# Kernel tuning notes

Measured on AMD Instinct MI355X. Metric: run time of the kernel, lower is better.

The kernel has to match this reference:

```python
import jax, jax.numpy as jnp
import numpy as np

B, T, V, F, H, WIN = 512, 49, 34, 16, 64, 4
W = T - WIN + 1  # 46 sliding windows


def make_pe(max_len, d):
    pos = np.arange(max_len, dtype=np.float32)[:, None]
    div = np.exp(np.arange(0, d, 2, dtype=np.float32) * (-np.log(10000.0) / d))
    pe = np.zeros((max_len, d), dtype=np.float32)
    pe[:, 0::2] = np.sin(pos * div)
    pe[:, 1::2] = np.cos(pos * div)
    return jnp.asarray(pe)


def impute(arr, delta_ts, mask, w, b):
    # arr/mask [B,T,V], delta_ts [B,T]; serial masked cumulative-sum + LOCF scan
    missing = (mask == 0).astype(arr.dtype)
    dd = jnp.broadcast_to(delta_ts[:, :, None], arr.shape)

    def step(carry, inp):
        c_prev, x_prev = carry
        d_t, x_t, m_t = inp
        c_t = d_t + c_prev * m_t                      # cum delta resets at observations
        x_new = jnp.where(m_t > 0, x_prev, x_t)       # last-observation carry-forward
        return (c_t, x_new), (c_t, x_new)

    xs = (dd.swapaxes(0, 1)[1:], arr.swapaxes(0, 1)[1:], missing.swapaxes(0, 1)[1:])
    _, (c_rest, x_rest) = jax.lax.scan(step, (dd[:, 0], arr[:, 0]), xs)
    cum = jnp.concatenate([dd[:, :1], c_rest.swapaxes(0, 1)], axis=1)
    last = jnp.concatenate([arr[:, :1], x_rest.swapaxes(0, 1)], axis=1)
    cum = cum / jnp.max(cum)
    decay = jnp.exp(-jnp.clip(w * cum + b, 0.0, 1000.0))  # w,b broadcast [1,V]
    means = jnp.mean(arr, axis=1, keepdims=True)
    return arr * mask + (1 - mask) * (decay * last + (1 - decay) * means)


def gru_layer(x, Wih, Whh, bih, bhh):
    # torch GRU gate order r,z,n; Wih [in,3H], Whh [H,3H]
    nB = x.shape[0]
    Hh = Whh.shape[0]
    xW = x @ Wih + bih  # [B,T,3H] precomputed input projections

    def step(h, xw_t):
        gh = h @ Whh + bhh
        xr, xz, xn = jnp.split(xw_t, 3, axis=-1)
        hr, hz, hn = jnp.split(gh, 3, axis=-1)
        r = jax.nn.sigmoid(xr + hr)
        z = jax.nn.sigmoid(xz + hz)
        n = jnp.tanh(xn + r * hn)
        h_new = (1 - z) * n + z * h
        return h_new, h_new

    _, ys = jax.lax.scan(step, jnp.zeros((nB, Hh), x.dtype), xW.swapaxes(0, 1))
    return ys.swapaxes(0, 1)


def forward(arr, mask, time, w_input_decay, b_input_decay,
            enc_W1, enc_b1, enc_W2, enc_b2,
            tla_Wq, tla_bq, tla_Wk, tla_bk, tla_Wv, tla_bv,
            adj, mp_W1, mp_b1, mp_W2, mp_b2,
            sa_Wq, sa_bq, sa_Wk, sa_bk, sa_Wv, sa_bv,
            gru_Wih0, gru_Whh0, gru_bih0, gru_bhh0,
            gru_Wih1, gru_Whh1, gru_bih1, gru_bhh1,
            ta_Wq, ta_bq, ta_Wk, ta_bk, ta_Wv, ta_bv,
            cls_W1, cls_b1, cls_W2, cls_b2):
    tt = time.T  # [B,T]
    delta = jnp.concatenate([jnp.zeros((tt.shape[0], 1), tt.dtype), tt[:, 1:] - tt[:, :-1]], axis=1)
    x = impute(arr, delta, mask, w_input_decay, b_input_decay)  # [B,T,V]
    # per-variable 2-layer MLP encoders (batched over V via einsum)
    inp = jnp.stack([x, mask], axis=-1)  # [B,T,V,2]
    h = jax.nn.relu(jnp.einsum('btvi,vif->btvf', inp, enc_W1) + enc_b1)
    enc = jnp.einsum('btvf,vfg->btvg', h, enc_W2) + enc_b2  # [B,T,V,F]
    # sliding windows (torch unfold + permute) + window positional encoding
    idx = jnp.arange(W)[:, None] + jnp.arange(WIN)[None, :]
    win = enc[:, idx] + make_pe(WIN, F)[None, None, :, None, :]
    xw = win.reshape(B * W, WIN, V, F)
    # TimeLagAttentionLayer: separate attention per variable, batched via einsum
    q = jnp.einsum('blvf,vfg->blvg', xw, tla_Wq) + tla_bq
    k = jnp.einsum('blvf,vfg->blvg', xw, tla_Wk) + tla_bk
    v = jnp.einsum('blvf,vfg->blvg', xw, tla_Wv) + tla_bv
    scores = jnp.einsum('blvg,bmvg->bvlm', q, k) / jnp.sqrt(jnp.asarray(F, xw.dtype))
    att = jax.nn.softmax(scores, axis=-1)
    att_out = jnp.einsum('bvlm,bmvf->bvf', att, v)  # (att @ v) then sum over lag dim
    # MessagePassingLayer
    message = jnp.einsum('uv,bvf->buf', adj, att_out)
    mp_out = jax.nn.relu(message @ mp_W1 + mp_b1) @ mp_W2 + mp_b2  # [B*W,V,1] (t_out path)
    _ = mp_out
    latent = message
    l_out = latent.reshape(B, W, V, F).transpose(0, 2, 3, 1)  # [B,V,F,W]
    # SignalAttentionLayer (faithful: permute to [B,V,W,F] then raw reshape to [B*W,V,F])
    xs = l_out + make_pe(V, F)[None, :, :, None]
    xs = xs.transpose(0, 1, 3, 2).reshape(B * W, V, F)
    Q = xs @ sa_Wq + sa_bq
    K = xs @ sa_Wk + sa_bk
    Vv = xs @ sa_Wv + sa_bv
    sw = jax.nn.softmax(jnp.einsum('bnd,bmd->bnm', Q, K) / jnp.sqrt(jnp.asarray(F, xs.dtype)), axis=-1)
    s_out = jnp.einsum('bnm,bmd->bd', sw, Vv).reshape(B, W, F)  # (w @ V).sum(dim=1)
    # 2-layer GRU predictor
    g1 = gru_layer(s_out, gru_Wih0, gru_Whh0, gru_bih0, gru_bhh0)
    g2 = gru_layer(g1, gru_Wih1, gru_Whh1, gru_bih1, gru_bhh1)  # [B,W,H]
    # TemporalAttention pooling
    xt = g2 + make_pe(W, H)[None]
    Qt = xt @ ta_Wq + ta_bq
    Kt = xt @ ta_Wk + ta_bk
    Vt = xt @ ta_Wv + ta_bv
    tw = jax.nn.softmax(jnp.einsum('bld,bmd->blm', Qt, Kt) / jnp.sqrt(jnp.asarray(H, xt.dtype)), axis=-1)
    t_val = jnp.einsum('blm,bmd->bd', tw, Vt)  # [B,H]
    pred = jax.nn.relu(t_val @ cls_W1 + cls_b1) @ cls_W2 + cls_b2  # [B,1]
    return pred


def setup_inputs():
    key = jax.random.key(0)
    ks = jax.random.split(key, 48)

    def rn(k, shape, s=0.1):
        return jax.random.normal(k, shape, jnp.float32) * s

    d = {}
    d['arr'] = jax.random.normal(ks[0], (B, T, V), jnp.float32)
    d['mask'] = (jax.random.uniform(ks[1], (B, T, V)) < 0.7).astype(jnp.float32)
    d['time'] = jnp.cumsum(jax.random.uniform(ks[2], (T, B), jnp.float32), axis=0)
    d['w_input_decay'] = jnp.full((1, V), 0.1, jnp.float32)
    d['b_input_decay'] = jnp.zeros((1, V), jnp.float32)
    d['enc_W1'] = rn(ks[3], (V, 2, F), 0.5); d['enc_b1'] = rn(ks[4], (V, F))
    d['enc_W2'] = rn(ks[5], (V, F, F), 0.25); d['enc_b2'] = rn(ks[6], (V, F))
    d['tla_Wq'] = rn(ks[7], (V, F, F), 0.25); d['tla_bq'] = rn(ks[8], (V, F))
    d['tla_Wk'] = rn(ks[9], (V, F, F), 0.25); d['tla_bk'] = rn(ks[10], (V, F))
    d['tla_Wv'] = rn(ks[11], (V, F, F), 0.25); d['tla_bv'] = rn(ks[12], (V, F))
    d['adj'] = jnp.eye(V, dtype=jnp.float32) + 0.2 * jnp.ones((V, V), jnp.float32)
    d['mp_W1'] = rn(ks[13], (F, F), 0.25); d['mp_b1'] = rn(ks[14], (F,))
    d['mp_W2'] = rn(ks[15], (F, 1), 0.25); d['mp_b2'] = rn(ks[16], (1,))
    d['sa_Wq'] = rn(ks[17], (F, F), 0.25); d['sa_bq'] = rn(ks[18], (F,))
    d['sa_Wk'] = rn(ks[19], (F, F), 0.25); d['sa_bk'] = rn(ks[20], (F,))
    d['sa_Wv'] = rn(ks[21], (F, F), 0.25); d['sa_bv'] = rn(ks[22], (F,))
    d['gru_Wih0'] = rn(ks[23], (F, 3 * H), 0.2); d['gru_Whh0'] = rn(ks[24], (H, 3 * H), 0.1)
    d['gru_bih0'] = rn(ks[25], (3 * H,)); d['gru_bhh0'] = rn(ks[26], (3 * H,))
    d['gru_Wih1'] = rn(ks[27], (H, 3 * H), 0.1); d['gru_Whh1'] = rn(ks[28], (H, 3 * H), 0.1)
    d['gru_bih1'] = rn(ks[29], (3 * H,)); d['gru_bhh1'] = rn(ks[30], (3 * H,))
    d['ta_Wq'] = rn(ks[31], (H, H), 0.12); d['ta_bq'] = rn(ks[32], (H,))
    d['ta_Wk'] = rn(ks[33], (H, H), 0.12); d['ta_bk'] = rn(ks[34], (H,))
    d['ta_Wv'] = rn(ks[35], (H, H), 0.12); d['ta_bv'] = rn(ks[36], (H,))
    d['cls_W1'] = rn(ks[37], (H, H), 0.12); d['cls_b1'] = rn(ks[38], (H,))
    d['cls_W2'] = rn(ks[39], (H, 1), 0.12); d['cls_b2'] = rn(ks[40], (1,))
    return d


def reference(arr, mask, time, w_input_decay, b_input_decay,
              enc_W1, enc_b1, enc_W2, enc_b2,
              tla_Wq, tla_bq, tla_Wk, tla_bk, tla_Wv, tla_bv,
              adj, mp_W1, mp_b1, mp_W2, mp_b2,
              sa_Wq, sa_bq, sa_Wk, sa_bk, sa_Wv, sa_bv,
              gru_Wih0, gru_Whh0, gru_bih0, gru_bhh0,
              gru_Wih1, gru_Whh1, gru_bih1, gru_bhh1,
              ta_Wq, ta_bq, ta_Wk, ta_bk, ta_Wv, ta_bv,
              cls_W1, cls_b1, cls_W2, cls_b2):
    return forward(arr, mask, time, w_input_decay, b_input_decay,
                   enc_W1, enc_b1, enc_W2, enc_b2,
                   tla_Wq, tla_bq, tla_Wk, tla_bk, tla_Wv, tla_bv,
                   adj, mp_W1, mp_b1, mp_W2, mp_b2,
                   sa_Wq, sa_bq, sa_Wk, sa_bk, sa_Wv, sa_bv,
                   gru_Wih0, gru_Whh0, gru_bih0, gru_bhh0,
                   gru_Wih1, gru_Whh1, gru_bih1, gru_bhh1,
                   ta_Wq, ta_bq, ta_Wk, ta_bk, ta_Wv, ta_bv,
                   cls_W1, cls_b1, cls_W2, cls_b2)
```

## Files before the change

kernel.cpp:

```cpp
#include <hip/hip_runtime.h>
#include <math.h>

#define BB 512
#define TT 49
#define VV 34
#define FF 16
#define HH 64
#define WW 46
#define BW (BB*WW)
#define TH3 (3*HH)
#define ROWS 25088
#define SG 2

#define SOUT_OFF   0ull
#define XW1_OFF    376832ull
#define G1_OFF     (XW1_OFF + 4521984ull)
#define XW2_OFF    (G1_OFF + 1507328ull)
#define G2_OFF     (XW2_OFF + 4521984ull)

#define MSG_SZ     12812288ull
#define CUM_SZ     852992ull
#define MEANS_SZ   17408ull
#define AO_OFF     12435456ull
#define MSG2_OFF   (AO_OFF + MSG_SZ)
#define CUM2_OFF   (MSG2_OFF + MSG_SZ)
#define LAST2_OFF  (CUM2_OFF + CUM_SZ)
#define MEANS2_OFF (LAST2_OFF + CUM_SZ)
#define MAX2_OFF   (MEANS2_OFF + MEANS_SZ)
#define PQ_OFF     (MAX2_OFF + 4ull)
#define SAW_OFF    (PQ_OFF + 6528ull)
#define FW_OFF     (SAW_OFF + 292ull)
#define WVIH_OFF   (FW_OFF + 27744ull)
#define BIAS2_OFF  (WVIH_OFF + 3072ull)

__global__ __launch_bounds__(256) void k_scan(
    const float* __restrict__ arr, const float* __restrict__ msk,
    const float* __restrict__ timeTB,
    float* __restrict__ cum, float* __restrict__ last,
    float* __restrict__ means, unsigned int* __restrict__ maxv) {
  int tid = blockIdx.x * 256 + threadIdx.x;
  int b = tid / VV, v = tid - b * VV;
  const int base = b * TT * VV + v;
  float x = arr[base];
  float c = 0.f, lm = 0.f, s = x;
  cum[base] = 0.f;
  last[base] = x;
  float tp = timeTB[b];
  for (int t = 1; t < TT; ++t) {
    float tc = timeTB[t * BB + b];
    float d = tc - tp; tp = tc;
    int e = base + t * VV;
    float a = arr[e], m = msk[e];
    float miss = (m == 0.f) ? 1.f : 0.f;
    c = d + c * miss;
    x = (miss > 0.f) ? x : a;
    cum[e] = c; last[e] = x;
    lm = fmaxf(lm, c);
    s += a;
  }
  means[tid] = s * (1.f / 49.f);
  #pragma unroll
  for (int off = 32; off; off >>= 1) lm = fmaxf(lm, __shfl_xor(lm, off));
  if ((threadIdx.x & 63) == 0) atomicMax(maxv, __float_as_uint(lm));
}

__global__ __launch_bounds__(256) void k_prep(
    const float* __restrict__ tlaWq, const float* __restrict__ tlaWk,
    const float* __restrict__ tlaWv,
    const float* __restrict__ tlaBq, const float* __restrict__ tlaBk,
    const float* __restrict__ tlaBv,
    const float* __restrict__ saWq, const float* __restrict__ saBq,
    const float* __restrict__ saWk, const float* __restrict__ saBk,
    const float* __restrict__ saWv, const float* __restrict__ saBv,
    const float* __restrict__ encW2, const float* __restrict__ encB2,
    const float* __restrict__ Wih0, const float* __restrict__ bih0,
    float* __restrict__ pqg, float* __restrict__ saw, float* __restrict__ fw,
    float* __restrict__ wvih, float* __restrict__ bias2) {
  const int bid = blockIdx.x;
  const int t = threadIdx.x;
  if (bid < 26) {
    int idx = bid * 256 + t;
    if (idx >= 6528) return;
    int which = idx / 2176;
    int r = idx - which * 2176;
    int l = r / 544;
    int rr = r - l * 544;
    int v = rr >> 4, f = rr & 15;
    const float* W = which == 0 ? tlaWq : which == 1 ? tlaWk : tlaWv;
    float acc = 0.f;
    #pragma unroll
    for (int i = 0; i < FF; ++i) {
      int i2 = i & ~1;
      float dv = expf(-logf(10000.f) * (float)i2 / (float)FF);
      float ang = (float)l * dv;
      float pe = (i & 1) ? cosf(ang) : sinf(ang);
      acc += pe * W[v * 256 + i * 16 + f];
    }
    pqg[idx] = acc;
  } else if (bid == 26) {
    int i = t & 15, j = t >> 4;
    float a = 0.f;
    #pragma unroll
    for (int f = 0; f < 16; ++f) a += saWq[i * 16 + f] * saWk[j * 16 + f];
    saw[j * 16 + i] = a;
    if (t < 16) {
      float pp = 0.f, qq = 0.f;
      #pragma unroll
      for (int f = 0; f < 16; ++f) { pp += saWq[t * 16 + f] * saBk[f]; qq += saWk[t * 16 + f] * saBq[f]; }
      saw[256 + t] = pp;
      saw[272 + t] = qq;
    }
    if (t == 0) {
      float c = 0.f;
      #pragma unroll
      for (int f = 0; f < 16; ++f) c += saBq[f] * saBk[f];
      saw[288] = c;
    }
  } else if (bid < 61) {
    const int v = bid - 27;
    const int f = t >> 4, o = t & 15;
    const float* W2v = encW2 + v * 256;
    float cq = 0.f, ck = 0.f, cv = 0.f;
    #pragma unroll
    for (int g = 0; g < 16; ++g) {
      float w2 = W2v[f * 16 + g];
      cq += w2 * tlaWq[v * 256 + g * 16 + o];
      ck += w2 * tlaWk[v * 256 + g * 16 + o];
      cv += w2 * tlaWv[v * 256 + g * 16 + o];
    }
    fw[v * 816 + 0 * 272 + f * 16 + o] = cq;
    fw[v * 816 + 1 * 272 + f * 16 + o] = ck;
    fw[v * 816 + 2 * 272 + f * 16 + o] = cv;
    if (t < 48) {
      int which = t >> 4, o2 = t & 15;
      const float* Wp = which == 0 ? tlaWq : which == 1 ? tlaWk : tlaWv;
      const float* Bp = which == 0 ? tlaBq : which == 1 ? tlaBk : tlaBv;
      float acc = Bp[v * 16 + o2];
      #pragma unroll
      for (int g = 0; g < 16; ++g) acc += encB2[v * 16 + g] * Wp[v * 256 + g * 16 + o2];
      fw[v * 816 + which * 272 + 256 + o2] = acc;
    }
  } else if (bid < 73) {
    int idx = (bid - 61) * 256 + t;
    int i = idx / 192, o = idx - i * 192;
    float acc = 0.f;
    #pragma unroll
    for (int f = 0; f < 16; ++f) acc += saWv[i * 16 + f] * Wih0[f * 192 + o];
    wvih[idx] = acc;
  } else {
    if (t < 192) {
      float acc = bih0[t];
      #pragma unroll
      for (int f = 0; f < 16; ++f) acc += 34.f * saBv[f] * Wih0[f * 192 + t];
      bias2[t] = acc;
    }
  }
}

__global__ __launch_bounds__(256) void k_enc4(
    const float* __restrict__ arr, const float* __restrict__ msk,
    const float* __restrict__ cum, const float* __restrict__ last,
    const float* __restrict__ means, const unsigned int* __restrict__ maxv,
    const float* __restrict__ wdec, const float* __restrict__ bdec,
    const float* __restrict__ W1, const float* __restrict__ B1,
    const float* __restrict__ fw, const float* __restrict__ pqg,
    float* __restrict__ ao) {
  __shared__ float pkv[4][3][TT * 17];
  const int v = blockIdx.x % VV;
  const int bgrp = blockIdx.x / VV;
  const int tid = threadIdx.x;
  const int wave = tid >> 6, lane = tid & 63;
  const int b = bgrp * 4 + wave;
  const float* fv = fw + v * 816;
  if (lane < TT) {
    const int t = lane;
    const int idx = (b * TT + t) * VV + v;
    float inv = 1.f / __uint_as_float(*maxv);
    float a = arr[idx], m = msk[idx];
    float cc = cum[idx] * inv;
    float ttc = fminf(fmaxf(wdec[v] * cc + bdec[v], 0.f), 1000.f);
    float dec = expf(-ttc);
    float xx = a * m + (1.f - m) * (dec * last[idx] + (1.f - dec) * means[b * VV + v]);
    float h[16];
    #pragma unroll
    for (int f = 0; f < 16; ++f)
      h[f] = fmaxf(xx * W1[v * 32 + f] + m * W1[v * 32 + 16 + f] + B1[v * 16 + f], 0.f);
    #pragma unroll
    for (int which = 0; which < 3; ++which) {
      const float* C = fv + which * 272;
      #pragma unroll
      for (int g = 0; g < 16; ++g) {
        float acc = C[256 + g];
        #pragma unroll
        for (int f = 0; f < 16; ++f) acc += h[f] * C[f * 16 + g];
        pkv[wave][which][t * 17 + g] = acc;
      }
    }
  }
  __syncthreads();
  if (lane < WW) {
    const int w = lane;
    const float* P = &pkv[wave][0][0];
    const float* K = &pkv[wave][1][0];
    const float* Vp = &pkv[wave][2][0];
    float kk[4][16];
    #pragma unroll
    for (int m = 0; m < 4; ++m)
      #pragma unroll
      for (int f = 0; f < 16; ++f)
        kk[m][f] = K[(w + m) * 17 + f] + pqg[2176 + m * 544 + v * 16 + f];
    float sc[4][4];
    #pragma unroll
    for (int l = 0; l < 4; ++l) {
      float qv[16];
      #pragma unroll
      for (int i = 0; i < 16; ++i)
        qv[i] = P[(w + l) * 17 + i] + pqg[l * 544 + v * 16 + i];
      #pragma unroll
      for (int m = 0; m < 4; ++m) {
        float s = 0.f;
        #pragma unroll
        for (int i = 0; i < 16; ++i) s += qv[i] * kk[m][i];
        sc[l][m] = s * 0.25f;
      }
    }
    float csum[4] = {0.f, 0.f, 0.f, 0.f};
    #pragma unroll
    for (int l = 0; l < 4; ++l) {
      float mx = fmaxf(fmaxf(sc[l][0], sc[l][1]), fmaxf(sc[l][2], sc[l][3]));
      float sum = 0.f;
      #pragma unroll
      for (int m = 0; m < 4; ++m) { sc[l][m] = expf(sc[l][m] - mx); sum += sc[l][m]; }
      float r = 1.f / sum;
      #pragma unroll
      for (int m = 0; m < 4; ++m) csum[m] += sc[l][m] * r;
    }
    float outv[16];
    #pragma unroll
    for (int f = 0; f < 16; ++f) outv[f] = 0.f;
    #pragma unroll
    for (int m = 0; m < 4; ++m) {
      float c = csum[m];
      #pragma unroll
      for (int f = 0; f < 16; ++f)
        outv[f] += c * (Vp[(w + m) * 17 + f] + pqg[2 * 2176 + m * 544 + v * 16 + f]);
    }
    float4* d4 = (float4*)(ao + ((size_t)(b * VV + v) * WW + w) * 16);
    #pragma unroll
    for (int j = 0; j < 4; ++j)
      d4[j] = make_float4(outv[4*j], outv[4*j+1], outv[4*j+2], outv[4*j+3]);
  }
}

#define MPW 12
__global__ __launch_bounds__(256) void k_mp(
    const float* __restrict__ ao, const float* __restrict__ adj,
    float* __restrict__ msg2) {
  __shared__ float adjs[VV * VV];
  __shared__ __align__(16) float aos[VV][MPW * 16];
  __shared__ float pes[VV * 16];
  const int bb = blockIdx.x >> 2;
  const int wt = blockIdx.x & 3;
  const int w0 = wt * MPW;
  const int wc = (wt == 3) ? (WW - 3 * MPW) : MPW;
  const int tid = threadIdx.x;
  for (int i = tid; i < VV * VV; i += 256) adjs[i] = adj[i];
  for (int i = tid; i < VV * 16; i += 256) {
    int u = i >> 4, f = i & 15;
    int f2 = f & ~1;
    float dv = expf(-logf(10000.f) * (float)f2 / 16.f);
    float ang = (float)u * dv;
    pes[i] = (f & 1) ? cosf(ang) : sinf(ang);
  }
  const int nq = wc * 4;
  for (int i = tid; i < VV * nq; i += 256) {
    int vv2 = i / nq, r = i - vv2 * nq;
    int wl = r >> 2, q = r & 3;
    float4 val = *(const float4*)(ao + ((size_t)(bb * VV + vv2) * WW + w0 + wl) * 16 + q * 4);
    *(float4*)&aos[vv2][wl * 16 + q * 4] = val;
  }
  __syncthreads();
  for (int i = tid; i < VV * nq; i += 256) {
    int u = i / nq, r = i - u * nq;
    int wl = r >> 2, q = r & 3;
    float a0 = 0.f, a1 = 0.f, a2 = 0.f, a3 = 0.f;
    for (int vv2 = 0; vv2 < VV; ++vv2) {
      float a = adjs[u * VV + vv2];
      float4 s = *(const float4*)&aos[vv2][wl * 16 + q * 4];
      a0 += a * s.x; a1 += a * s.y; a2 += a * s.z; a3 += a * s.w;
    }
    float4 o = make_float4(a0 + pes[u * 16 + q * 4],
                           a1 + pes[u * 16 + q * 4 + 1],
                           a2 + pes[u * 16 + q * 4 + 2],
                           a3 + pes[u * 16 + q * 4 + 3]);
    *(float4*)(msg2 + ((size_t)(bb * VV + u) * WW + w0 + wl) * 16 + q * 4) = o;
  }
}

#define DOT4(a,b) ((a).x*(b).x + (a).y*(b).y + (a).z*(b).z + (a).w*(b).w)
__global__ __launch_bounds__(256) void k_sa4(
    const float* __restrict__ msg2, const float* __restrict__ saw,
    const float* __restrict__ wvih, const float* __restrict__ bias2,
    float* __restrict__ xw1) {
  __shared__ float As[256];
  __shared__ float ps[16], q2s[16];
  __shared__ __align__(16) float xs[SG][36][20];
  __shared__ __align__(16) float zs[SG][36][20];
  __shared__ float sc[SG][36][37];
  __shared__ float uws[SG][36], vws[SG][36];
  __shared__ float rs[SG][34], cs[SG][34];
  __shared__ float ys[SG][16];
  __shared__ float c0s;
  const int tid = threadIdx.x;
  const int n0 = blockIdx.x * SG;
  As[tid] = saw[tid];
  if (tid < 16) { ps[tid] = saw[256 + tid]; q2s[tid] = saw[272 + tid]; }
  if (tid == 0) c0s = saw[288];
  {
    const float4* src = (const float4*)(msg2 + (size_t)n0 * 544);
    for (int i = tid; i < SG * 136; i += 256) {
      int g = i / 136, r = i - g * 136;
      int m = r >> 2, q = r & 3;
      ((float4*)&xs[g][m][0])[q] = src[i];
    }
  }
  __syncthreads();
  for (int idx = tid; idx < SG * 136; idx += 256) {
    int g = idx / 136, r = idx - g * 136;
    int m0 = (r >> 3) * 2, i0 = (r & 7) * 2;
    float z00 = 0.f, z01 = 0.f, z10 = 0.f, z11 = 0.f;
    #pragma unroll
    for (int jc = 0; jc < 4; ++jc) {
      float4 xa = ((const float4*)&xs[g][m0][0])[jc];
      float4 xb = ((const float4*)&xs[g][m0 + 1][0])[jc];
      #pragma unroll
      for (int jj = 0; jj < 4; ++jj) {
        int j = jc * 4 + jj;
        float xj0 = (jj == 0) ? xa.x : (jj == 1) ? xa.y : (jj == 2) ? xa.z : xa.w;
        float xj1 = (jj == 0) ? xb.x : (jj == 1) ? xb.y : (jj == 2) ? xb.z : xb.w;
        float a0 = As[j * 16 + i0], a1 = As[j * 16 + i0 + 1];
        z00 += a0 * xj0; z01 += a1 * xj0; z10 += a0 * xj1; z11 += a1 * xj1;
      }
    }
    zs[g][m0][i0] = z00; zs[g][m0][i0 + 1] = z01;
    zs[g][m0 + 1][i0] = z10; zs[g][m0 + 1][i0 + 1] = z11;
  }
  if (tid < SG * 34) {
    int g = tid / 34, m = tid - g * 34;
    float pu = 0.f, pv = 0.f;
    #pragma unroll
    for (int i = 0; i < 16; ++i) { float x = xs[g][m][i]; pu += x * ps[i]; pv += x * q2s[i]; }
    uws[g][m] = pu; vws[g][m] = pv;
  }
  __syncthreads();
  for (int idx = tid; idx < SG * 81; idx += 256) {
    int g = idx / 81, r = idx - g * 81;
    int l0 = (r / 9) * 4, m0 = (r - (r / 9) * 9) * 4;
    float s00=0,s01=0,s02=0,s03=0, s10=0,s11=0,s12=0,s13=0;
    float s20=0,s21=0,s22=0,s23=0, s30=0,s31=0,s32=0,s33=0;
    #pragma unroll
    for (int ic = 0; ic < 4; ++ic) {
      float4 x0 = ((const float4*)&xs[g][l0 + 0][0])[ic];
      float4 x1 = ((const float4*)&xs[g][l0 + 1][0])[ic];
      float4 x2 = ((const float4*)&xs[g][l0 + 2][0])[ic];
      float4 x3 = ((const float4*)&xs[g][l0 + 3][0])[ic];
      float4 z0 = ((const float4*)&zs[g][m0 + 0][0])[ic];
      float4 z1 = ((const float4*)&zs[g][m0 + 1][0])[ic];
      float4 z2 = ((const float4*)&zs[g][m0 + 2][0])[ic];
      float4 z3 = ((const float4*)&zs[g][m0 + 3][0])[ic];
      s00 += DOT4(x0,z0); s01 += DOT4(x0,z1); s02 += DOT4(x0,z2); s03 += DOT4(x0,z3);
      s10 += DOT4(x1,z0); s11 += DOT4(x1,z1); s12 += DOT4(x1,z2); s13 += DOT4(x1,z3);
      s20 += DOT4(x2,z0); s21 += DOT4(x2,z1); s22 += DOT4(x2,z2); s23 += DOT4(x2,z3);
      s30 += DOT4(x3,z0); s31 += DOT4(x3,z1); s32 += DOT4(x3,z2); s33 += DOT4(x3,z3);
    }
    float c0 = c0s;
    float u0 = uws[g][l0], u1 = uws[g][l0+1], u2 = uws[g][l0+2], u3 = uws[g][l0+3];
    float v0 = vws[g][m0], v1 = vws[g][m0+1], v2 = vws[g][m0+2], v3 = vws[g][m0+3];
    sc[g][l0+0][m0+0] = (s00+u0+v0+c0)*0.25f; sc[g][l0+0][m0+1] = (s01+u0+v1+c0)*0.25f;
    sc[g][l0+0][m0+2] = (s02+u0+v2+c0)*0.25f; sc[g][l0+0][m0+3] = (s03+u0+v3+c0)*0.25f;
    sc[g][l0+1][m0+0] = (s10+u1+v0+c0)*0.25f; sc[g][l0+1][m0+1] = (s11+u1+v1+c0)*0.25f;
    sc[g][l0+1][m0+2] = (s12+u1+v2+c0)*0.25f; sc[g][l0+1][m0+3] = (s13+u1+v3+c0)*0.25f;
    sc[g][l0+2][m0+0] = (s20+u2+v0+c0)*0.25f; sc[g][l0+2][m0+1] = (s21+u2+v1+c0)*0.25f;
    sc[g][l0+2][m0+2] = (s22+u2+v2+c0)*0.25f; sc[g][l0+2][m0+3] = (s23+u2+v3+c0)*0.25f;
    sc[g][l0+3][m0+0] = (s30+u3+v0+c0)*0.25f; sc[g][l0+3][m0+1] = (s31+u3+v1+c0)*0.25f;
    sc[g][l0+3][m0+2] = (s32+u3+v2+c0)*0.25f; sc[g][l0+3][m0+3] = (s33+u3+v3+c0)*0.25f;
  }
  __syncthreads();
  if (tid < SG * 34) {
    int g = tid / 34, l = tid - g * 34;
    float mx = -1e30f;
    for (int m = 0; m < 34; ++m) mx = fmaxf(mx, sc[g][l][m]);
    float sum = 0.f;
    for (int m = 0; m < 34; ++m) { float e = expf(sc[g][l][m] - mx); sc[g][l][m] = e; sum += e; }
    rs[g][l] = 1.f / sum;
  }
  __syncthreads();
  if (tid < SG * 34) {
    int g = tid / 34, m = tid - g * 34;
    float acc = 0.f;
    for (int l = 0; l < 34; ++l) acc += sc[g][l][m] * rs[g][l];
    cs[g][m] = acc;
  }
  __syncthreads();
  if (tid < SG * 16) {
    int g = tid >> 4, i = tid & 15;
    float acc = 0.f;
    for (int m = 0; m < 34; ++m) acc += cs[g][m] * xs[g][m][i];
    ys[g][i] = acc;
  }
  __syncthreads();
  for (int idx = tid; idx < SG * 192; idx += 256) {
    int g = idx / 192, o = idx - g * 192;
    float acc = bias2[o];
    #pragma unroll
    for (int i = 0; i < 16; ++i) acc += ys[g][i] * wvih[i * 192 + o];
    xw1[(size_t)(n0 + g) * 192 + o] = acc;
  }
}

#define RL(x,i) __uint_as_float(__builtin_amdgcn_readlane(__float_as_uint(x), (i)))
__global__ __launch_bounds__(64) void k_gru2(
    const float* __restrict__ xw, const float* __restrict__ Whh,
    const float* __restrict__ bhh, float* __restrict__ gout) {
  const int tid = threadIdx.x;
  const int b = blockIdx.x;
  float wr[64], wz[64], wn[64];
  #pragma unroll
  for (int i = 0; i < 64; ++i) {
    wr[i] = Whh[i * 192 + tid];
    wz[i] = Whh[i * 192 + 64 + tid];
    wn[i] = Whh[i * 192 + 128 + tid];
  }
  const float br = bhh[tid], bz = bhh[64 + tid], bn = bhh[128 + tid];
  float h = 0.f;
  const float* xr = xw + (size_t)b * WW * 192;
  for (int w = 0; w < WW; ++w, xr += 192) {
    float xrv = xr[tid], xzv = xr[64 + tid], xnv = xr[128 + tid];
    float pr0 = br, pr1 = 0.f, pr2 = 0.f, pr3 = 0.f;
    float pz0 = bz, pz1 = 0.f, pz2 = 0.f, pz3 = 0.f;
    float pn0 = bn, pn1 = 0.f, pn2 = 0.f, pn3 = 0.f;
    #pragma unroll
    for (int i = 0; i < 64; i += 4) {
      float h0 = RL(h, i), h1 = RL(h, i + 1), h2 = RL(h, i + 2), h3 = RL(h, i + 3);
      pr0 += h0 * wr[i];     pr1 += h1 * wr[i + 1];
      pr2 += h2 * wr[i + 2]; pr3 += h3 * wr[i + 3];
      pz0 += h0 * wz[i];     pz1 += h1 * wz[i + 1];
      pz2 += h2 * wz[i + 2]; pz3 += h3 * wz[i + 3];
      pn0 += h0 * wn[i];     pn1 += h1 * wn[i + 1];
      pn2 += h2 * wn[i + 2]; pn3 += h3 * wn[i + 3];
    }
    float ar = (pr0 + pr1) + (pr2 + pr3);
    float az = (pz0 + pz1) + (pz2 + pz3);
    float an = (pn0 + pn1) + (pn2 + pn3);
    float r = 1.f / (1.f + expf(-(xrv + ar)));
    float z = 1.f / (1.f + expf(-(xzv + az)));
    float n = tanhf(xnv + r * an);
    h = (1.f - z) * n + z * h;
    gout[((size_t)b * WW + w) * HH + tid] = h;
  }
}

__global__ __launch_bounds__(192) void k_xw2(
    const float* __restrict__ x, const float* __restrict__ Wih,
    const float* __restrict__ bih, float* __restrict__ xw) {
  __shared__ float xsh[16][HH];
  int n0 = blockIdx.x * 16;
  int tid = threadIdx.x;
  for (int idx = tid; idx < 16 * HH; idx += 192) {
    int ns = idx >> 6, i = idx & 63;
    xsh[ns][i] = x[(size_t)(n0 + ns) * HH + i];
  }
  __syncthreads();
  float acc[16];
  float bb = bih[tid];
  #pragma unroll
  for (int ns = 0; ns < 16; ++ns) acc[ns] = bb;
  for (int i = 0; i < HH; ++i) {
    float wv = Wih[i * TH3 + tid];
    #pragma unroll
    for (int ns = 0; ns < 16; ++ns) acc[ns] += xsh[ns][i] * wv;
  }
  #pragma unroll
  for (int ns = 0; ns < 16; ++ns) xw[(size_t)(n0 + ns) * TH3 + tid] = acc[ns];
}

__global__ __launch_bounds__(256) void k_ta(
    const float* __restrict__ g2,
    const float* __restrict__ Wq, const float* __restrict__ bq,
    const float* __restrict__ Wk, const float* __restrict__ bk,
    const float* __restrict__ Wv, const float* __restrict__ bv,
    const float* __restrict__ cW1, const float* __restrict__ cb1,
    const float* __restrict__ cW2, const float* __restrict__ cb2,
    float* __restrict__ out) {
  __shared__ float xt[WW * 65];
  __shared__ float QKVs[3][WW * 65];
  __shared__ float sc[WW * WW];
  __shared__ float cs[WW];
  __shared__ float tval[HH];
  __shared__ float hrelu[HH];
  int tid = threadIdx.x;
  int b = blockIdx.x;
  for (int idx = tid; idx < WW * HH; idx += 256) {
    int w = idx >> 6, d = idx & 63;
    int f2 = d & ~1;
    float dv = expf(-logf(10000.f) * (float)f2 / (float)HH);
    float ang = (float)w * dv;
    float pe = (d & 1) ? cosf(ang) : sinf(ang);
    xt[w * 65 + d] = g2[(size_t)(b * WW + w) * HH + d] + pe;
  }
  __syncthreads();
  if (tid < 192) {
    int which = tid >> 6, d = tid & 63;
    const float* Wt = which == 0 ? Wq : which == 1 ? Wk : Wv;
    float bias = (which == 0 ? bq : which == 1 ? bk : bv)[d];
    float col[HH];
    #pragma unroll
    for (int i = 0; i < HH; ++i) col[i] = Wt[i * HH + d];
    float* dst = &QKVs[which][0];
    for (int w = 0; w < WW; ++w) {
      float acc = bias;
      #pragma unroll
      for (int i = 0; i < HH; ++i) acc += xt[w * 65 + i] * col[i];
      dst[w * 65 + d] = acc;
    }
  }
  __syncthreads();
  for (int idx = tid; idx < WW * WW; idx += 256) {
    int l = idx / WW, m = idx - l * WW;
    float s = 0.f;
    #pragma unroll
    for (int i = 0; i < HH; ++i) s += QKVs[0][l * 65 + i] * QKVs[1][m * 65 + i];
    sc[idx] = s * 0.125f;
  }
  __syncthreads();
  if (tid < WW) {
    float mx = -1e30f;
    for (int m = 0; m < WW; ++m) mx = fmaxf(mx, sc[tid * WW + m]);
    float sum = 0.f;
    for (int m = 0; m < WW; ++m) { float e = expf(sc[tid * WW + m] - mx); sc[tid * WW + m] = e; sum += e; }
    float r = 1.f / sum;
    for (int m = 0; m < WW; ++m) sc[tid * WW + m] *= r;
  }
  __syncthreads();
  if (tid < WW) {
    float s = 0.f;
    for (int l = 0; l < WW; ++l) s += sc[l * WW + tid];
    cs[tid] = s;
  }
  __syncthreads();
  if (tid < HH) {
    float acc = 0.f;
    for (int m = 0; m < WW; ++m) acc += cs[m] * QKVs[2][m * 65 + tid];
    tval[tid] = acc;
  }
  __syncthreads();
  if (tid < HH) {
    float acc = cb1[tid];
    #pragma unroll
    for (int d = 0; d < HH; ++d) acc += tval[d] * cW1[d * HH + tid];
    hrelu[tid] = fmaxf(acc, 0.f);
  }
  __syncthreads();
  if (tid == 0) {
    float acc = cb2[0];
    for (int j = 0; j < HH; ++j) acc += hrelu[j] * cW2[j];
    out[b] = acc;
  }
}

extern "C" void kernel_launch(void* const* d_in, const int* in_sizes, int n_in,
                              void* d_out, int out_size, void* d_ws, size_t ws_size,
                              hipStream_t stream) {
  (void)in_sizes; (void)n_in; (void)out_size; (void)ws_size;
  const float* arr    = (const float*)d_in[0];
  const float* msk    = (const float*)d_in[1];
  const float* timeTB = (const float*)d_in[2];
  const float* wdec   = (const float*)d_in[3];
  const float* bdec   = (const float*)d_in[4];
  const float* encW1  = (const float*)d_in[5];
  const float* encB1  = (const float*)d_in[6];
  const float* encW2  = (const float*)d_in[7];
  const float* encB2  = (const float*)d_in[8];
  const float* tlaWq  = (const float*)d_in[9];
  const float* tlaBq  = (const float*)d_in[10];
  const float* tlaWk  = (const float*)d_in[11];
  const float* tlaBk  = (const float*)d_in[12];
  const float* tlaWv  = (const float*)d_in[13];
  const float* tlaBv  = (const float*)d_in[14];
  const float* adj    = (const float*)d_in[15];
  const float* saWq   = (const float*)d_in[20];
  const float* saBq   = (const float*)d_in[21];
  const float* saWk   = (const float*)d_in[22];
  const float* saBk   = (const float*)d_in[23];
  const float* saWv   = (const float*)d_in[24];
  const float* saBv   = (const float*)d_in[25];
  const float* gWih0  = (const float*)d_in[26];
  const float* gWhh0  = (const float*)d_in[27];
  const float* gBih0  = (const float*)d_in[28];
  const float* gBhh0  = (const float*)d_in[29];
  const float* gWih1  = (const float*)d_in[30];
  const float* gWhh1  = (const float*)d_in[31];
  const float* gBih1  = (const float*)d_in[32];
  const float* gBhh1  = (const float*)d_in[33];
  const float* taWq   = (const float*)d_in[34];
  const float* taBq   = (const float*)d_in[35];
  const float* taWk   = (const float*)d_in[36];
  const float* taBk   = (const float*)d_in[37];
  const float* taWv   = (const float*)d_in[38];
  const float* taBv   = (const float*)d_in[39];
  const float* cW1    = (const float*)d_in[40];
  const float* cb1    = (const float*)d_in[41];
  const float* cW2    = (const float*)d_in[42];
  const float* cb2    = (const float*)d_in[43];
  float* out = (float*)d_out;
  float* ws  = (float*)d_ws;

  float* ao    = ws + AO_OFF;
  float* msg2  = ws + MSG2_OFF;
  float* cum   = ws + CUM2_OFF;
  float* last  = ws + LAST2_OFF;
  float* means = ws + MEANS2_OFF;
  unsigned int* maxv = (unsigned int*)(ws + MAX2_OFF);
  float* pqg   = ws + PQ_OFF;
  float* saw   = ws + SAW_OFF;
  float* fw    = ws + FW_OFF;
  float* wvih  = ws + WVIH_OFF;
  float* bias2 = ws + BIAS2_OFF;

  float* xw1  = ws + XW1_OFF;
  float* g1   = ws + G1_OFF;
  float* xw2  = ws + XW2_OFF;
  float* g2   = ws + G2_OFF;

  hipMemsetAsync(maxv, 0, sizeof(unsigned int), stream);
  k_scan<<<68, 256, 0, stream>>>(arr, msk, timeTB, cum, last, means, maxv);
  k_prep<<<74, 256, 0, stream>>>(tlaWq, tlaWk, tlaWv, tlaBq, tlaBk, tlaBv,
                                 saWq, saBq, saWk, saBk, saWv, saBv,
                                 encW2, encB2, gWih0, gBih0,
                                 pqg, saw, fw, wvih, bias2);
  k_enc4<<<VV * 128, 256, 0, stream>>>(arr, msk, cum, last, means, maxv,
                                       wdec, bdec, encW1, encB1, fw, pqg, ao);
  k_mp<<<BB * 4, 256, 0, stream>>>(ao, adj, msg2);
  k_sa4<<<BW / SG, 256, 0, stream>>>(msg2, saw, wvih, bias2, xw1);
  k_gru2<<<BB, 64, 0, stream>>>(xw1, gWhh0, gBhh0, g1);
  k_xw2<<<BW / 16, 192, 0, stream>>>(g1, gWih1, gBih1, xw2);
  k_gru2<<<BB, 64, 0, stream>>>(xw2, gWhh1, gBhh1, g2);
  k_ta<<<BB, 256, 0, stream>>>(g2, taWq, taBq, taWk, taBk, taWv, taBv,
                               cW1, cb1, cW2, cb2, out);
}
```

Measured before the change: 347.1 us.

## Restructure spatial attention kernel to one wavefront per window with register rows

Replaces the SG=2 shared-memory tiled spatial-attention kernel with a version that handles four windows per block, one wavefront per window. Each lane owns one query row: it computes the projected row z, the scores against all 34 keys and the softmax entirely in registers, then writes only the normalized probabilities to LDS. Weights are read directly from global memory (uniform loads) instead of being staged in shared memory. This cuts block count and barrier-separated phases, and fuses the softmax normalization into the score loop. In exchange, lanes 34-63 sit idle during most phases and register pressure rises from the 16+34 float arrays per lane.

```diff
diff --git a/kernel.cpp b/kernel.cpp
--- a/kernel.cpp
+++ b/kernel.cpp
@@ -10,7 +10,6 @@
 #define BW (BB*WW)
 #define TH3 (3*HH)
 #define ROWS 25088
-#define SG 2
 
 #define SOUT_OFF   0ull
 #define XW1_OFF    376832ull
@@ -297,124 +296,104 @@
   }
 }
 
-#define DOT4(a,b) ((a).x*(b).x + (a).y*(b).y + (a).z*(b).z + (a).w*(b).w)
-__global__ __launch_bounds__(256) void k_sa4(
+__global__ __launch_bounds__(256) void k_sa5(
     const float* __restrict__ msg2, const float* __restrict__ saw,
     const float* __restrict__ wvih, const float* __restrict__ bias2,
     float* __restrict__ xw1) {
-  __shared__ float As[256];
-  __shared__ float ps[16], q2s[16];
-  __shared__ __align__(16) float xs[SG][36][20];
-  __shared__ __align__(16) float zs[SG][36][20];
-  __shared__ float sc[SG][36][37];
-  __shared__ float uws[SG][36], vws[SG][36];
-  __shared__ float rs[SG][34], cs[SG][34];
-  __shared__ float ys[SG][16];
-  __shared__ float c0s;
+  __shared__ __align__(16) float xs[4][VV * 20];
+  __shared__ float esc[4][VV * 35];
+  __shared__ float wsL[4][VV];
+  __shared__ float csL[4][VV];
+  __shared__ __align__(16) float ybL[4][16];
   const int tid = threadIdx.x;
-  const int n0 = blockIdx.x * SG;
-  As[tid] = saw[tid];
-  if (tid < 16) { ps[tid] = saw[256 + tid]; q2s[tid] = saw[272 + tid]; }
-  if (tid == 0) c0s = saw[288];
+  const int g = tid >> 6, lane = tid & 63;
+  const int n = blockIdx.x * 4 + g;
   {
-    const float4* src = (const float4*)(msg2 + (size_t)n0 * 544);
-    for (int i = tid; i < SG * 136; i += 256) {
-      int g = i / 136, r = i - g * 136;
+    const float4* src = (const float4*)(msg2 + (size_t)blockIdx.x * 4 * 544);
+    for (int i = tid; i < 544; i += 256) {
+      int gg = i / 136, r = i - gg * 136;
       int m = r >> 2, q = r & 3;
-      ((float4*)&xs[g][m][0])[q] = src[i];
-    }
-  }
-  __syncthreads();
-  for (int idx = tid; idx < SG * 136; idx += 256) {
-    int g = idx / 136, r = idx - g * 136;
-    int m0 = (r >> 3) * 2, i0 = (r & 7) * 2;
-    float z00 = 0.f, z01 = 0.f, z10 = 0.f, z11 = 0.f;
-    #pragma unroll
-    for (int jc = 0; jc < 4; ++jc) {
-      float4 xa = ((const float4*)&xs[g][m0][0])[jc];
-      float4 xb = ((const float4*)&xs[g][m0 + 1][0])[jc];
-      #pragma unroll
-      for (int jj = 0; jj < 4; ++jj) {
-        int j = jc * 4 + jj;
-        float xj0 = (jj == 0) ? xa.x : (jj == 1) ? xa.y : (jj == 2) ? xa.z : xa.w;
-        float xj1 = (jj == 0) ? xb.x : (jj == 1) ? xb.y : (jj == 2) ? xb.z : xb.w;
-        float a0 = As[j * 16 + i0], a1 = As[j * 16 + i0 + 1];
-        z00 += a0 * xj0; z01 += a1 * xj0; z10 += a0 * xj1; z11 += a1 * xj1;
-      }
-    }
-    zs[g][m0][i0] = z00; zs[g][m0][i0 + 1] = z01;
-    zs[g][m0 + 1][i0] = z10; zs[g][m0 + 1][i0 + 1] = z11;
-  }
-  if (tid < SG * 34) {
-    int g = tid / 34, m = tid - g * 34;
-    float pu = 0.f, pv = 0.f;
-    #pragma unroll
-    for (int i = 0; i < 16; ++i) { float x = xs[g][m][i]; pu += x * ps[i]; pv += x * q2s[i]; }
-    uws[g][m] = pu; vws[g][m] = pv;
-  }
-  __syncthreads();
-  for (int idx = tid; idx < SG * 81; idx += 256) {
-    int g = idx / 81, r = idx - g * 81;
-    int l0 = (r / 9) * 4, m0 = (r - (r / 9) * 9) * 4;
-    float s00=0,s01=0,s02=0,s03=0, s10=0,s11=0,s12=0,s13=0;
-    float s20=0,s21=0,s22=0,s23=0, s30=0,s31=0,s32=0,s33=0;
-    #pragma unroll
-    for (int ic = 0; ic < 4; ++ic) {
-      float4 x0 = ((const float4*)&xs[g][l0 + 0][0])[ic];
-      float4 x1 = ((const float4*)&xs[g][l0 + 1][0])[ic];
-      float4 x2 = ((const float4*)&xs[g][l0 + 2][0])[ic];
-      float4 x3 = ((const float4*)&xs[g][l0 + 3][0])[ic];
-      float4 z0 = ((const float4*)&zs[g][m0 + 0][0])[ic];
-      float4 z1 = ((const float4*)&zs[g][m0 + 1][0])[ic];
-      float4 z2 = ((const float4*)&zs[g][m0 + 2][0])[ic];
-      float4 z3 = ((const float4*)&zs[g][m0 + 3][0])[ic];
-      s00 += DOT4(x0,z0); s01 += DOT4(x0,z1); s02 += DOT4(x0,z2); s03 += DOT4(x0,z3);
-      s10 += DOT4(x1,z0); s11 += DOT4(x1,z1); s12 += DOT4(x1,z2); s13 += DOT4(x1,z3);
-      s20 += DOT4(x2,z0); s21 += DOT4(x2,z1); s22 += DOT4(x2,z2); s23 += DOT4(x2,z3);
-      s30 += DOT4(x3,z0); s31 += DOT4(x3,z1); s32 += DOT4(x3,z2); s33 += DOT4(x3,z3);
-    }
-    float c0 = c0s;
-    float u0 = uws[g][l0], u1 = uws[g][l0+1], u2 = uws[g][l0+2], u3 = uws[g][l0+3];
-    float v0 = vws[g][m0], v1 = vws[g][m0+1], v2 = vws[g][m0+2], v3 = vws[g][m0+3];
-    sc[g][l0+0][m0+0] = (s00+u0+v0+c0)*0.25f; sc[g][l0+0][m0+1] = (s01+u0+v1+c0)*0.25f;
-    sc[g][l0+0][m0+2] = (s02+u0+v2+c0)*0.25f; sc[g][l0+0][m0+3] = (s03+u0+v3+c0)*0.25f;
-    sc[g][l0+1][m0+0] = (s10+u1+v0+c0)*0.25f; sc[g][l0+1][m0+1] = (s11+u1+v1+c0)*0.25f;
-    sc[g][l0+1][m0+2] = (s12+u1+v2+c0)*0.25f; sc[g][l0+1][m0+3] = (s13+u1+v3+c0)*0.25f;
-    sc[g][l0+2][m0+0] = (s20+u2+v0+c0)*0.25f; sc[g][l0+2][m0+1] = (s21+u2+v1+c0)*0.25f;
-    sc[g][l0+2][m0+2] = (s22+u2+v2+c0)*0.25f; sc[g][l0+2][m0+3] = (s23+u2+v3+c0)*0.25f;
-    sc[g][l0+3][m0+0] = (s30+u3+v0+c0)*0.25f; sc[g][l0+3][m0+1] = (s31+u3+v1+c0)*0.25f;
-    sc[g][l0+3][m0+2] = (s32+u3+v2+c0)*0.25f; sc[g][l0+3][m0+3] = (s33+u3+v3+c0)*0.25f;
-  }
-  __syncthreads();
-  if (tid < SG * 34) {
-    int g = tid / 34, l = tid - g * 34;
-    float mx = -1e30f;
-    for (int m = 0; m < 34; ++m) mx = fmaxf(mx, sc[g][l][m]);
+      ((float4*)&xs[gg][m * 20])[q] = src[i];
+    }
+  }
+  __syncthreads();
+  float z[16];
+  float u = 0.f;
+  if (lane < VV) {
+    float x[16];
+    const float4* xr = (const float4*)&xs[g][lane * 20];
+    float4 a0 = xr[0], a1 = xr[1], a2 = xr[2], a3 = xr[3];
+    x[0]=a0.x; x[1]=a0.y; x[2]=a0.z; x[3]=a0.w;
+    x[4]=a1.x; x[5]=a1.y; x[6]=a1.z; x[7]=a1.w;
+    x[8]=a2.x; x[9]=a2.y; x[10]=a2.z; x[11]=a2.w;
+    x[12]=a3.x; x[13]=a3.y; x[14]=a3.z; x[15]=a3.w;
+    #pragma unroll
+    for (int j = 0; j < 16; ++j) {
+      float acc = 0.f;
+      #pragma unroll
+      for (int i = 0; i < 16; ++i) acc += saw[j * 16 + i] * x[i];
+      z[j] = acc;
+    }
+    float w = 0.f;
+    #pragma unroll
+    for (int i = 0; i < 16; ++i) { u += saw[256 + i] * x[i]; w += saw[272 + i] * x[i]; }
+    wsL[g][lane] = w;
+  }
+  __syncthreads();
+  if (lane < VV) {
+    const float c0 = saw[288];
+    float e[VV];
+    #pragma unroll
+    for (int m = 0; m < VV; ++m) {
+      const float4* xm = (const float4*)&xs[g][m * 20];
+      float4 b0 = xm[0], b1 = xm[1], b2 = xm[2], b3 = xm[3];
+      float p0 = z[0]*b0.x + z[1]*b0.y + z[2]*b0.z + z[3]*b0.w;
+      float p1 = z[4]*b1.x + z[5]*b1.y + z[6]*b1.z + z[7]*b1.w;
+      float p2 = z[8]*b2.x + z[9]*b2.y + z[10]*b2.z + z[11]*b2.w;
+      float p3 = z[12]*b3.x + z[13]*b3.y + z[14]*b3.z + z[15]*b3.w;
+      e[m] = (((p0 + p1) + (p2 + p3)) + u + wsL[g][m] + c0) * 0.25f;
+    }
+    float mx = e[0];
+    #pragma unroll
+    for (int m = 1; m < VV; ++m) mx = fmaxf(mx, e[m]);
     float sum = 0.f;
-    for (int m = 0; m < 34; ++m) { float e = expf(sc[g][l][m] - mx); sc[g][l][m] = e; sum += e; }
-    rs[g][l] = 1.f / sum;
-  }
-  __syncthreads();
-  if (tid < SG * 34) {
-    int g = tid / 34, m = tid - g * 34;
+    #pragma unroll
+    for (int m = 0; m < VV; ++m) { e[m] = expf(e[m] - mx); sum += e[m]; }
+    float rr = 1.f / sum;
+    #pragma unroll
+    for (int m = 0; m < VV; ++m) esc[g][lane * 35 + m] = e[m] * rr;
+  }
+  __syncthreads();
+  if (lane < VV) {
+    float cs = 0.f;
+    #pragma unroll
+    for (int l = 0; l < VV; ++l) cs += esc[g][l * 35 + lane];
+    csL[g][lane] = cs;
+  }
+  __syncthreads();
+  if (lane < 16) {
     float acc = 0.f;
-    for (int l = 0; l < 34; ++l) acc += sc[g][l][m] * rs[g][l];
-    cs[g][m] = acc;
-  }
-  __syncthreads();
-  if (tid < SG * 16) {
-    int g = tid >> 4, i = tid & 15;
-    float acc = 0.f;
-    for (int m = 0; m < 34; ++m) acc += cs[g][m] * xs[g][m][i];
-    ys[g][i] = acc;
-  }
-  __syncthreads();
-  for (int idx = tid; idx < SG * 192; idx += 256) {
-    int g = idx / 192, o = idx - g * 192;
-    float acc = bias2[o];
-    #pragma unroll
-    for (int i = 0; i < 16; ++i) acc += ys[g][i] * wvih[i * 192 + o];
-    xw1[(size_t)(n0 + g) * 192 + o] = acc;
+    #pragma unroll
+    for (int m = 0; m < VV; ++m) acc += csL[g][m] * xs[g][m * 20 + lane];
+    ybL[g][lane] = acc;
+  }
+  __syncthreads();
+  {
+    const float4* yr = (const float4*)&ybL[g][0];
+    float4 y0 = yr[0], y1 = yr[1], y2 = yr[2], y3 = yr[3];
+    float yv[16];
+    yv[0]=y0.x; yv[1]=y0.y; yv[2]=y0.z; yv[3]=y0.w;
+    yv[4]=y1.x; yv[5]=y1.y; yv[6]=y1.z; yv[7]=y1.w;
+    yv[8]=y2.x; yv[9]=y2.y; yv[10]=y2.z; yv[11]=y2.w;
+    yv[12]=y3.x; yv[13]=y3.y; yv[14]=y3.z; yv[15]=y3.w;
+    #pragma unroll
+    for (int k = 0; k < 3; ++k) {
+      int o = lane + k * 64;
+      float acc = bias2[o];
+      #pragma unroll
+      for (int i = 0; i < 16; ++i) acc += yv[i] * wvih[i * 192 + o];
+      xw1[(size_t)n * 192 + o] = acc;
+    }
   }
 }
 
@@ -641,7 +620,7 @@
   k_enc4<<<VV * 128, 256, 0, stream>>>(arr, msk, cum, last, means, maxv,
                                        wdec, bdec, encW1, encB1, fw, pqg, ao);
   k_mp<<<BB * 4, 256, 0, stream>>>(ao, adj, msg2);
-  k_sa4<<<BW / SG, 256, 0, stream>>>(msg2, saw, wvih, bias2, xw1);
+  k_sa5<<<BW / 4, 256, 0, stream>>>(msg2, saw, wvih, bias2, xw1);
   k_gru2<<<BB, 64, 0, stream>>>(xw1, gWhh0, gBhh0, g1);
   k_xw2<<<BW / 16, 192, 0, stream>>>(g1, gWih1, gBih1, xw2);
   k_gru2<<<BB, 64, 0, stream>>>(xw2, gWhh1, gBhh1, g2);
```

Measured after the change: 338.1 us. 1.03x faster.
